# Optimization experiments

Measured on AMD Instinct MI355X. Metric: run time of the kernel, lower is better.

## Reference

```python
import jax, jax.numpy as jnp
import numpy as np

B, T, W = 8, 4096, 1024          # batch, byte seq len, words per sequence
DB, DW = 64, 512                 # byte_embed_dim, word_embed_dim
NH = 2                           # highway layers per block
VOCAB = 264                      # 256 bytes + 4 + 4 specials
BPE_MARK, WORD_MARK = 4, 3       # bpe_mask_idx, word_mask_idx


def _make_seg_ids():
    # ragged word lengths in {3,4,5}, mean 4, summing to T per sequence
    rng = np.random.default_rng(0)
    seg = np.empty((B, T), np.int32)
    base = T // W
    for b in range(B):
        delta = np.zeros(W, np.int64)
        q = W // 4
        idx = rng.permutation(W)
        delta[idx[:q]] = 1
        delta[idx[q:2 * q]] = -1
        seg[b] = np.repeat(np.arange(W), base + delta)
    return jnp.asarray(seg)


def setup_inputs() -> dict:
    key = jax.random.key(0)
    ks = jax.random.split(key, 12)
    s = 0.05
    byte_tokens = jax.random.randint(ks[0], (B, T), 4, VOCAB)
    bpe_mask = jax.random.bernoulli(ks[1], 0.25, (B, T))
    word_mask = jax.random.bernoulli(ks[2], 0.05, (B, T))
    seg_ids = _make_seg_ids()
    tok_emb = (jax.random.normal(ks[3], (VOCAB, DB)) * s).at[0].set(0.0)  # padding_idx=0 row zeroed
    inp = {
        'byte_tokens': byte_tokens, 'bpe_mask': bpe_mask, 'word_mask': word_mask,
        'seg_ids': seg_ids, 'tok_emb': tok_emb,
        'conv0_w': jax.random.normal(ks[4], (3, DB, DW)) * s, 'conv0_b': jnp.zeros((DW,)),
        'hw0_wg': jax.random.normal(ks[5], (NH, DW, DW)) * s, 'hw0_bg': jnp.zeros((NH, DW)),
        'hw0_wh': jax.random.normal(ks[6], (NH, DW, DW)) * s, 'hw0_bh': jnp.zeros((NH, DW)),
        'conv1_w': jax.random.normal(ks[7], (3, DW, DW)) * s, 'conv1_b': jnp.zeros((DW,)),
        'hw1_wg': jax.random.normal(ks[8], (NH, DW, DW)) * s, 'hw1_bg': jnp.zeros((NH, DW)),
        'hw1_wh': jax.random.normal(ks[9], (NH, DW, DW)) * s, 'hw1_bh': jnp.zeros((NH, DW)),
        'proj_w': jax.random.normal(ks[10], (DW, DW)) * s, 'proj_b': jnp.zeros((DW,)),
    }
    return inp


def _conv_highway(x, cw, cb, wg, bg, wh, bh, residual):
    # 1D same-padded conv over sequence, optional residual, relu, then highways
    y = jax.lax.conv_general_dilated(x, cw, (1,), 'SAME',
                                     dimension_numbers=('NWC', 'WIO', 'NWC')) + cb
    if residual:
        y = y + x
    y = jax.nn.relu(y)
    for i in range(NH):
        g = jax.nn.sigmoid(y @ wg[i] + bg[i])
        h = jax.nn.relu(y @ wh[i] + bh[i])
        y = g * h + (1.0 - g) * y
    return y


def reference(byte_tokens, bpe_mask, word_mask, seg_ids, tok_emb,
              conv0_w, conv0_b, hw0_wg, hw0_bg, hw0_wh, hw0_bh,
              conv1_w, conv1_b, hw1_wg, hw1_bg, hw1_wh, hw1_bh,
              proj_w, proj_b):
    # byte embedding + marker embeddings (pad idx 0 -> zero row)
    x = (tok_emb[byte_tokens]
         + tok_emb[jnp.where(bpe_mask, BPE_MARK, 0)]
         + tok_emb[jnp.where(word_mask, WORD_MARK, 0)])          # [B,T,DB]
    x = _conv_highway(x, conv0_w, conv0_b, hw0_wg, hw0_bg, hw0_wh, hw0_bh, False)
    x = _conv_highway(x, conv1_w, conv1_b, hw1_wg, hw1_bg, hw1_wh, hw1_bh, True)
    # ragged per-word segment max over bytes (fused, replaces python loops)
    seg_max = jax.vmap(lambda xi, si: jax.ops.segment_max(xi, si, num_segments=W))
    x = seg_max(x, seg_ids)                                       # [B,W,DW]
    return x @ proj_w + proj_b
```

## Files before the change

kernel.cpp:

```cpp
#include <hip/hip_runtime.h>
#include <hip/hip_bf16.h>

using bf16 = __hip_bfloat16;
typedef __attribute__((ext_vector_type(8))) short s8v;
typedef __attribute__((ext_vector_type(4))) float f4v;

#define T_SEQ 4096
#define DWC 512

__device__ __forceinline__ float fin(float v) {
    return (v == v && fabsf(v) < 1e30f) ? v : 0.0f;
}
__device__ __forceinline__ float ldf(const void* p, size_t i, int f32) {
    return f32 ? ((const float*)p)[i] : __bfloat162float(((const bf16*)p)[i]);
}
__device__ __forceinline__ float b2f(short s) {
    unsigned u = ((unsigned)(unsigned short)s) << 16;
    return __builtin_bit_cast(float, u);
}
__device__ __forceinline__ short f2b(float v) {
    bf16 b = __float2bfloat16(v);
    return __builtin_bit_cast(short, b);
}
__device__ __forceinline__ uint4 ld16(const short* p) { return *(const uint4*)p; }

__device__ __forceinline__ void gl_lds16(const short* g, short* l) {
    __builtin_amdgcn_global_load_lds(
        (const __attribute__((address_space(1))) void*)g,
        (__attribute__((address_space(3))) void*)l, 16, 0, 0);
}

__device__ __forceinline__ void swz(int L, int G, int& bx, int& by) {
    int k8 = L & 7, sl = L >> 3;
    int gp = G >> 5;
    bx = sl & 3;
    by = k8 * gp + (sl >> 2);
}

__device__ __forceinline__ int swidx(int row, int ch) {
    return row * 32 + ((ch ^ ((row >> 1) & 3)) << 3);
}

__global__ __launch_bounds__(256) void diag_kernel(bf16* __restrict__ out, int n, float v)
{
    int i = blockIdx.x * 256 + threadIdx.x;
    if (i < n) out[i] = __float2bfloat16(i == 0 ? v : 0.0f);
}

__global__ __launch_bounds__(256) void detect_kernel(
    const int* __restrict__ tok, const unsigned char* __restrict__ bpe,
    const unsigned char* __restrict__ wm, const int* __restrict__ seg,
    const unsigned int* __restrict__ embw, int* __restrict__ flags)
{
    __shared__ int sh[5];
    int tid = threadIdx.x;
    if (tid < 5) sh[tid] = 0;
    __syncthreads();
    int bo = 0, bm = 0, wo = 0, wmid = 0;
    for (int i = tid; i < 16384; i += 256) {
        int odd = 2 * i + 1;
        if (bpe[odd]) bo = 1;
        if (wm[odd])  wo = 1;
        int mid = 8 * (i & 4095) + 4;
        if (bpe[mid]) bm = 1;
        if (wm[mid])  wmid = 1;
    }
    if (bo)   atomicOr(&sh[0], 1);
    if (bm)   atomicOr(&sh[1], 1);
    if (wo)   atomicOr(&sh[2], 1);
    if (wmid) atomicOr(&sh[3], 1);
    if (tid < 32 && embw[32 + tid] != 0u) atomicOr(&sh[4], 1);
    __syncthreads();
    if (tid == 0) {
        flags[0] = (tok[32767] != 0) ? 0 : 1;
        flags[1] = sh[0] ? 1 : (sh[1] ? 4 : 8);
        flags[2] = sh[2] ? 1 : (sh[3] ? 4 : 8);
        flags[3] = (seg[32767] != 0) ? 0 : 1;
        flags[4] = sh[4] ? 0 : 1;
    }
}

#define WB_TOTAL 3249664
#define EMB4_ELEMS (264 * 4 * 64)
__global__ __launch_bounds__(256) void convert_weights(
    const void* c0w, const void* c0b, const void* h0g, const void* h0bg,
    const void* h0h, const void* h0bh, const void* c1w, const void* c1b,
    const void* h1g, const void* h1bg, const void* h1h, const void* h1bh,
    const void* pw, const void* pb, const void* emb,
    const int* __restrict__ flags, short* __restrict__ WB)
{
    int f32 = flags[4];
    size_t i = (size_t)blockIdx.x * 256 + threadIdx.x;
    if (i >= WB_TOTAL + EMB4_ELEMS) return;
    if (i >= WB_TOTAL) {
        size_t o = i - WB_TOTAL;
        size_t t = o >> 8, v = (o >> 6) & 3, c = o & 63;
        float val = ldf(emb, t * 64 + c, f32);
        if (v & 1) val += ldf(emb, 4 * 64 + c, f32);
        if (v & 2) val += ldf(emb, 3 * 64 + c, f32);
        WB[i] = f2b(fin(val));
        return;
    }
    const void* src; size_t si;
    if (i < 98304)        { size_t n = i / 192, k = i % 192; src = c0w; si = k * 512 + n; }
    else if (i < 98816)   { src = c0b;  si = i - 98304; }
    else if (i < 623104)  { size_t o = i - 98816;  size_t l = o >> 18; o &= 262143;
                            size_t n = o >> 9, k = o & 511; src = h0g; si = (l << 18) + k * 512 + n; }
    else if (i < 624128)  { src = h0bg; si = i - 623104; }
    else if (i < 1148416) { size_t o = i - 624128; size_t l = o >> 18; o &= 262143;
                            size_t n = o >> 9, k = o & 511; src = h0h; si = (l << 18) + k * 512 + n; }
    else if (i < 1149440) { src = h0bh; si = i - 1148416; }
    else if (i < 1935872) { size_t o = i - 1149440; size_t n = o / 1536, k = o % 1536;
                            src = c1w; si = k * 512 + n; }
    else if (i < 1936384) { src = c1b;  si = i - 1935872; }
    else if (i < 2460672) { size_t o = i - 1936384; size_t l = o >> 18; o &= 262143;
                            size_t n = o >> 9, k = o & 511; src = h1g; si = (l << 18) + k * 512 + n; }
    else if (i < 2461696) { src = h1bg; si = i - 2460672; }
    else if (i < 2985984) { size_t o = i - 2461696; size_t l = o >> 18; o &= 262143;
                            size_t n = o >> 9, k = o & 511; src = h1h; si = (l << 18) + k * 512 + n; }
    else if (i < 2987008) { src = h1bh; si = i - 2985984; }
    else if (i < 3249152) { size_t o = i - 2987008; size_t n = o >> 9, k = o & 511;
                            src = pw; si = k * 512 + n; }
    else                  { src = pb;   si = i - 3249152; }
    WB[i] = f2b(ldf(src, si, f32));
}

__global__ __launch_bounds__(512) void conv0_mfma(
    const int* __restrict__ tok, const unsigned char* __restrict__ bpe,
    const unsigned char* __restrict__ wm, const short* __restrict__ emb4,
    const int* __restrict__ flags, const short* __restrict__ WT,
    const short* __restrict__ bias, short* __restrict__ Out)
{
    constexpr int K = 192;
    constexpr int NIT = 3;
    __shared__ __align__(16) short As[2][256 * 32];
    __shared__ __align__(16) short Bs[2][256 * 32];
    int bx, by;
    swz(blockIdx.x, gridDim.x, bx, by);
    const int bm = by * 128, bn = bx * 128;
    const int tid = threadIdx.x;
    const int wave = tid >> 6, lane = tid & 63;
    const int wmr = (wave >> 1) * 32, wnc = (wave & 1) * 64;
    const int q = lane >> 4, ln16 = lane & 15;
    const int sr = tid >> 2, sch = tid & 3;
    const int tt = (bm + sr) & (T_SEQ - 1);
    const int is64t = flags[0];
    const int wb = flags[1], ww = flags[2];
    const short* Bb = WT + (size_t)(bn + sr) * K + sch * 8;

    f4v acc[2][4] = {};
    uint4 rA0, rA1, rB0, rB1;
    const uint4 z4 = make_uint4(0, 0, 0, 0);

    auto loadA = [&](int tap, uint4& a0, uint4& a1) {
        int ts = tt + tap - 1;
        if ((unsigned)ts < (unsigned)T_SEQ) {
            int bt = bm + sr + tap - 1;
            int tk = is64t ? (int)((const long long*)tok)[bt] : tok[bt];
            tk = min(max(tk, 0), 263);
            int v = (bpe[(size_t)bt * wb] ? 1 : 0) | (wm[(size_t)bt * ww] ? 2 : 0);
            const short* row = emb4 + ((size_t)tk * 4 + v) * 64;
            a0 = ld16(row + sch * 8);
            a1 = ld16(row + 32 + sch * 8);
        } else { a0 = z4; a1 = z4; }
    };

    loadA(0, rA0, rA1);
    rB0 = ld16(Bb);
    rB1 = ld16(Bb + 32);
    *(uint4*)(&As[0][swidx(sr, sch)])       = rA0;
    *(uint4*)(&As[0][swidx(128 + sr, sch)]) = rA1;
    *(uint4*)(&Bs[0][swidx(sr, sch)])       = rB0;
    *(uint4*)(&Bs[0][swidx(128 + sr, sch)]) = rB1;
    __syncthreads();
    int p = 0;

    for (int it = 0; it < NIT; ++it) {
        const bool more = (it + 1 < NIT);
        if (more) {
            int kn = (it + 1) * 64;
            loadA(it + 1, rA0, rA1);
            rB0 = ld16(Bb + kn);
            rB1 = ld16(Bb + kn + 32);
        }
        #pragma unroll
        for (int ks = 0; ks < 2; ks++) {
            s8v af[2], bf[4];
            #pragma unroll
            for (int mi = 0; mi < 2; mi++)
                af[mi] = *(const s8v*)(&As[p][swidx(128 * ks + wmr + mi * 16 + ln16, q)]);
            #pragma unroll
            for (int ni = 0; ni < 4; ni++)
                bf[ni] = *(const s8v*)(&Bs[p][swidx(128 * ks + wnc + ni * 16 + ln16, q)]);
            #pragma unroll
            for (int mi = 0; mi < 2; mi++)
                #pragma unroll
                for (int ni = 0; ni < 4; ni++)
                    acc[mi][ni] = __builtin_amdgcn_mfma_f32_16x16x32_bf16(
                        af[mi], bf[ni], acc[mi][ni], 0, 0, 0);
        }
        if (more) {
            *(uint4*)(&As[p ^ 1][swidx(sr, sch)])       = rA0;
            *(uint4*)(&As[p ^ 1][swidx(128 + sr, sch)]) = rA1;
            *(uint4*)(&Bs[p ^ 1][swidx(sr, sch)])       = rB0;
            *(uint4*)(&Bs[p ^ 1][swidx(128 + sr, sch)]) = rB1;
            __syncthreads();
            p ^= 1;
        }
    }

    #pragma unroll
    for (int mi = 0; mi < 2; mi++)
        #pragma unroll
        for (int ni = 0; ni < 4; ni++) {
            int col = bn + wnc + ni * 16 + ln16;
            float bv = b2f(bias[col]);
            #pragma unroll
            for (int r = 0; r < 4; r++) {
                int orow = bm + wmr + mi * 16 + q * 4 + r;
                Out[(size_t)orow * DWC + col] =
                    f2b(fin(fmaxf(acc[mi][ni][r] + bv, 0.0f)));
            }
        }
}

__global__ __launch_bounds__(512) void conv1_mfma(
    const short* __restrict__ A, const short* __restrict__ WT,
    const short* __restrict__ bias, short* __restrict__ Out)
{
    constexpr int IC = 512;
    constexpr int K = 3 * IC;
    constexpr int NIT = K / 64;
    __shared__ __align__(16) short As[2][256 * 32];
    __shared__ __align__(16) short Bs[2][256 * 32];
    int bx, by;
    swz(blockIdx.x, gridDim.x, bx, by);
    const int bm = by * 128, bn = bx * 128;
    const int tid = threadIdx.x;
    const int wave = tid >> 6, lane = tid & 63;
    const int wmr = (wave >> 1) * 32, wnc = (wave & 1) * 64;
    const int q = lane >> 4, ln16 = lane & 15;
    const int sr = tid >> 2, sch = tid & 3;
    const int tt = (bm + sr) & (T_SEQ - 1);
    const short* Bb = WT + (size_t)(bn + sr) * K + sch * 8;

    f4v acc[2][4] = {};
    uint4 rA0, rA1, rB0, rB1;
    const uint4 z4 = make_uint4(0, 0, 0, 0);

    {
        int ts = tt - 1;
        bool ok = (ts >= 0 && ts < T_SEQ);
        const short* sa = A + (size_t)(bm + sr - 1) * IC + sch * 8;
        rA0 = ok ? ld16(sa) : z4;
        rA1 = ok ? ld16(sa + 32) : z4;
        rB0 = ld16(Bb);
        rB1 = ld16(Bb + 32);
    }
    *(uint4*)(&As[0][swidx(sr, sch)])       = rA0;
    *(uint4*)(&As[0][swidx(128 + sr, sch)]) = rA1;
    *(uint4*)(&Bs[0][swidx(sr, sch)])       = rB0;
    *(uint4*)(&Bs[0][swidx(128 + sr, sch)]) = rB1;
    __syncthreads();
    int p = 0;

    for (int it = 0; it < NIT; ++it) {
        const bool more = (it + 1 < NIT);
        if (more) {
            int kn = (it + 1) * 64;
            int tap = kn / IC, c0 = kn - tap * IC;
            int ts = tt + tap - 1;
            bool ok = (ts >= 0 && ts < T_SEQ);
            const short* sa = A + (size_t)(bm + sr + tap - 1) * IC + c0 + sch * 8;
            rA0 = ok ? ld16(sa) : z4;
            rA1 = ok ? ld16(sa + 32) : z4;
            rB0 = ld16(Bb + kn);
            rB1 = ld16(Bb + kn + 32);
        }
        #pragma unroll
        for (int ks = 0; ks < 2; ks++) {
            s8v af[2], bf[4];
            #pragma unroll
            for (int mi = 0; mi < 2; mi++)
                af[mi] = *(const s8v*)(&As[p][swidx(128 * ks + wmr + mi * 16 + ln16, q)]);
            #pragma unroll
            for (int ni = 0; ni < 4; ni++)
                bf[ni] = *(const s8v*)(&Bs[p][swidx(128 * ks + wnc + ni * 16 + ln16, q)]);
            #pragma unroll
            for (int mi = 0; mi < 2; mi++)
                #pragma unroll
                for (int ni = 0; ni < 4; ni++)
                    acc[mi][ni] = __builtin_amdgcn_mfma_f32_16x16x32_bf16(
                        af[mi], bf[ni], acc[mi][ni], 0, 0, 0);
        }
        if (more) {
            *(uint4*)(&As[p ^ 1][swidx(sr, sch)])       = rA0;
            *(uint4*)(&As[p ^ 1][swidx(128 + sr, sch)]) = rA1;
            *(uint4*)(&Bs[p ^ 1][swidx(sr, sch)])       = rB0;
            *(uint4*)(&Bs[p ^ 1][swidx(128 + sr, sch)]) = rB1;
            __syncthreads();
            p ^= 1;
        }
    }

    #pragma unroll
    for (int mi = 0; mi < 2; mi++)
        #pragma unroll
        for (int ni = 0; ni < 4; ni++) {
            int col = bn + wnc + ni * 16 + ln16;
            float bv = b2f(bias[col]);
            #pragma unroll
            for (int r = 0; r < 4; r++) {
                int orow = bm + wmr + mi * 16 + q * 4 + r;
                float v = acc[mi][ni][r] + bv + b2f(A[(size_t)orow * IC + col]);
                Out[(size_t)orow * DWC + col] = f2b(fin(fmaxf(v, 0.0f)));
            }
        }
}

__global__ __launch_bounds__(512, 4) void highway_mfma8(
    const short* __restrict__ Y, const short* __restrict__ WgT,
    const short* __restrict__ bg, const short* __restrict__ WhT,
    const short* __restrict__ bh, short* __restrict__ Out)
{
    constexpr int IC = DWC;
    constexpr int NIT = IC / 32;
    __shared__ __align__(16) short As [2][128 * 32];
    __shared__ __align__(16) short Bgs[2][128 * 32];
    __shared__ __align__(16) short Bhs[2][128 * 32];
    int bx, by;
    swz(blockIdx.x, gridDim.x, bx, by);
    const int bm = by * 128, bn = bx * 128;
    const int tid = threadIdx.x;
    const int wave = tid >> 6, lane = tid & 63;
    const int wmr = (wave >> 2) * 64;
    const int wnc = (wave & 3) * 32;
    const int q = lane >> 4, ln16 = lane & 15;

    const int rr = (wave << 4) + (lane >> 2);
    const int ch = (lane & 3) ^ ((rr >> 1) & 3);
    const short* gA = Y   + (size_t)(bm + rr) * IC + ch * 8;
    const short* gG = WgT + (size_t)(bn + rr) * IC + ch * 8;
    const short* gH = WhT + (size_t)(bn + rr) * IC + ch * 8;
    const int wb1k = wave << 10;

    f4v accg[4][2] = {};
    f4v acch[4][2] = {};

    auto stage = [&](int pp, int kk) {
        gl_lds16(gA + kk, (short*)((char*)&As [pp][0] + wb1k));
        gl_lds16(gG + kk, (short*)((char*)&Bgs[pp][0] + wb1k));
        gl_lds16(gH + kk, (short*)((char*)&Bhs[pp][0] + wb1k));
    };

    stage(0, 0);
    asm volatile("s_waitcnt vmcnt(0)" ::: "memory");
    __syncthreads();
    int p = 0;

    for (int it = 0; it < NIT; ++it) {
        const bool more = (it + 1 < NIT);
        if (more) stage(p ^ 1, (it + 1) * 32);
        const short* Ap = &As [p][0];
        const short* Gp = &Bgs[p][0];
        const short* Hp = &Bhs[p][0];
        s8v af[2], bgf[2], bhf[2];
        #pragma unroll
        for (int ni = 0; ni < 2; ni++) {
            bgf[ni] = *(const s8v*)(&Gp[swidx(wnc + ni * 16 + ln16, q)]);
            bhf[ni] = *(const s8v*)(&Hp[swidx(wnc + ni * 16 + ln16, q)]);
        }
        #pragma unroll
        for (int mh = 0; mh < 2; mh++) {
            #pragma unroll
            for (int mi = 0; mi < 2; mi++)
                af[mi] = *(const s8v*)(&Ap[swidx(wmr + mh * 32 + mi * 16 + ln16, q)]);
            #pragma unroll
            for (int mi = 0; mi < 2; mi++)
                #pragma unroll
                for (int ni = 0; ni < 2; ni++) {
                    accg[mh * 2 + mi][ni] = __builtin_amdgcn_mfma_f32_16x16x32_bf16(
                        af[mi], bgf[ni], accg[mh * 2 + mi][ni], 0, 0, 0);
                    acch[mh * 2 + mi][ni] = __builtin_amdgcn_mfma_f32_16x16x32_bf16(
                        af[mi], bhf[ni], acch[mh * 2 + mi][ni], 0, 0, 0);
                }
        }
        if (more) {
            asm volatile("s_waitcnt vmcnt(0)" ::: "memory");
            __builtin_amdgcn_s_barrier();
            p ^= 1;
        }
    }

    #pragma unroll
    for (int mi = 0; mi < 4; mi++)
        #pragma unroll
        for (int ni = 0; ni < 2; ni++) {
            int col = bn + wnc + ni * 16 + ln16;
            float bgv = b2f(bg[col]);
            float bhv = b2f(bh[col]);
            #pragma unroll
            for (int r = 0; r < 4; r++) {
                int orow = bm + wmr + mi * 16 + q * 4 + r;
                float g = 1.0f / (1.0f + expf(-(accg[mi][ni][r] + bgv)));
                float h = fmaxf(acch[mi][ni][r] + bhv, 0.0f);
                float yv = b2f(Y[(size_t)orow * DWC + col]);
                Out[(size_t)orow * DWC + col] = f2b(fin(g * h + (1.0f - g) * yv));
            }
        }
}

__global__ __launch_bounds__(512) void proj_mfma(
    const short* __restrict__ A, const short* __restrict__ WT,
    const short* __restrict__ bias, const int* __restrict__ flags,
    void* __restrict__ Out, int oroff)
{
    __shared__ __align__(16) short As[128 * 32];
    __shared__ __align__(16) short Bs[128 * 32];
    int bx, by;
    swz(blockIdx.x, gridDim.x, bx, by);
    const int bm = by * 128, bn = bx * 128;
    const int tid = threadIdx.x;
    const int wave = tid >> 6, lane = tid & 63;
    const int wmr = (wave >> 1) * 32, wnc = (wave & 1) * 64;
    const int q = lane >> 4, ln16 = lane & 15;
    const int sr = tid >> 2, sch = tid & 3;
    const int sw = swidx(sr, sch);
    const int f32 = flags[4];
    const short* A0 = A  + (size_t)(bm + sr) * DWC + sch * 8;
    const short* B0 = WT + (size_t)(bn + sr) * DWC + sch * 8;

    f4v acc[2][4] = {};
    uint4 rA = ld16(A0), rB = ld16(B0);

    for (int k0 = 0; k0 < DWC; k0 += 32) {
        *(uint4*)(&As[sw]) = rA;
        *(uint4*)(&Bs[sw]) = rB;
        __syncthreads();
        if (k0 + 32 < DWC) {
            int kn = k0 + 32;
            rA = ld16(A0 + kn); rB = ld16(B0 + kn);
        }
        s8v af[2], bf[4];
        #pragma unroll
        for (int mi = 0; mi < 2; mi++) af[mi] = *(const s8v*)(&As[swidx(wmr + mi * 16 + ln16, q)]);
        #pragma unroll
        for (int ni = 0; ni < 4; ni++) bf[ni] = *(const s8v*)(&Bs[swidx(wnc + ni * 16 + ln16, q)]);
        #pragma unroll
        for (int mi = 0; mi < 2; mi++)
            #pragma unroll
            for (int ni = 0; ni < 4; ni++)
                acc[mi][ni] = __builtin_amdgcn_mfma_f32_16x16x32_bf16(
                    af[mi], bf[ni], acc[mi][ni], 0, 0, 0);
        __syncthreads();
    }

    #pragma unroll
    for (int mi = 0; mi < 2; mi++)
        #pragma unroll
        for (int ni = 0; ni < 4; ni++) {
            int col = bn + wnc + ni * 16 + ln16;
            float bv = b2f(bias[col]);
            #pragma unroll
            for (int r = 0; r < 4; r++) {
                int orow = bm + wmr + mi * 16 + q * 4 + r;
                float v = fin(acc[mi][ni][r] + bv);
                size_t oi = (size_t)(oroff + orow) * DWC + col;
                if (f32) ((float*)Out)[oi] = v;
                else     ((bf16*)Out)[oi] = __float2bfloat16(v);
            }
        }
}

__global__ __launch_bounds__(256) void bounds_kernel(
    const int* __restrict__ seg, const int* __restrict__ flags,
    int* __restrict__ wstart, int* __restrict__ wend, int bt0)
{
    int il = blockIdx.x * 256 + threadIdx.x;
    int ig = bt0 + il;
    int is64 = flags[3];
    const long long* seg64 = (const long long*)seg;
    int t = il & (T_SEQ - 1);
    int bl = il >> 12;
    int s  = (is64 ? (int)seg64[ig] : seg[ig]) & 1023;
    int sp = (t == 0)         ? -1 : ((is64 ? (int)seg64[ig - 1] : seg[ig - 1]) & 1023);
    int sn = (t == T_SEQ - 1) ? -1 : ((is64 ? (int)seg64[ig + 1] : seg[ig + 1]) & 1023);
    int bw = (bl << 10) + s;
    if (sp != s) wstart[bw] = t;
    if (sn != s) wend[bw] = t;
}

__global__ __launch_bounds__(512) void segmax_kernel(
    const short* __restrict__ Y, const int* __restrict__ wstart,
    const int* __restrict__ wend, short* __restrict__ Out)
{
    int bw = blockIdx.x;
    int d = threadIdx.x;
    int bl = bw >> 10;
    int s = wstart[bw], e = wend[bw];
    s = min(max(s, 0), T_SEQ - 1);
    e = min(max(e, s), T_SEQ - 1);
    float m = b2f(Y[(size_t)((bl << 12) + s) * DWC + d]);
    for (int t = s + 1; t <= e; ++t)
        m = fmaxf(m, b2f(Y[(size_t)((bl << 12) + t) * DWC + d]));
    Out[(size_t)bw * DWC + d] = f2b(fin(m));
}

extern "C" void kernel_launch(void* const* d_in, const int* in_sizes, int n_in,
                              void* d_out, int out_size, void* d_ws, size_t ws_size,
                              hipStream_t stream)
{
    static const int expect[19] = {32768, 32768, 32768, 32768, 16896,
                                   98304, 512, 524288, 1024, 524288, 1024,
                                   786432, 512, 524288, 1024, 524288, 1024,
                                   262144, 512};
    int bad = -1;
    if (n_in < 19) bad = 31;
    else for (int i = 0; i < 19; i++) if (in_sizes[i] != expect[i]) { bad = i; break; }
    if (bad >= 0) {
        diag_kernel<<<dim3((out_size + 255) / 256), dim3(256), 0, stream>>>(
            (bf16*)d_out, out_size, 1e35f * (float)(1 + bad));
        return;
    }

    char* ws = (char*)d_ws;
    const size_t WBREG = 8ull << 20;
    short* WB    = (short*)ws;
    int*   flags = (int*)(ws + (7u << 20));
    const size_t perC = 8388608 + 8192 + 64;
    int C = 8;
    while (C > 1 && WBREG + (size_t)C * perC > ws_size) C >>= 1;
    if (WBREG + (size_t)C * perC > ws_size) {
        float ws_mib = (float)((double)ws_size / 1048576.0);
        diag_kernel<<<dim3((out_size + 255) / 256), dim3(256), 0, stream>>>(
            (bf16*)d_out, out_size, 1e30f * (16.0f + ws_mib));
        return;
    }

    const int*  byte_tokens = (const int*)d_in[0];
    const unsigned char* bpe_mask = (const unsigned char*)d_in[1];
    const unsigned char* word_mask = (const unsigned char*)d_in[2];
    const int*  seg_ids     = (const int*)d_in[3];
    const void* tok_emb = d_in[4];

    detect_kernel<<<dim3(1), dim3(256), 0, stream>>>(
        byte_tokens, bpe_mask, word_mask, seg_ids,
        (const unsigned int*)tok_emb, flags);

    convert_weights<<<dim3((WB_TOTAL + EMB4_ELEMS + 255) / 256), dim3(256), 0, stream>>>(
        d_in[5], d_in[6], d_in[7], d_in[8], d_in[9], d_in[10],
        d_in[11], d_in[12], d_in[13], d_in[14], d_in[15], d_in[16],
        d_in[17], d_in[18], tok_emb, flags, WB);

    short* c0wT = WB;            short* c0b  = WB + 98304;
    short* h0gT = WB + 98816;    short* h0bg = WB + 623104;
    short* h0hT = WB + 624128;   short* h0bh = WB + 1148416;
    short* c1wT = WB + 1149440;  short* c1b  = WB + 1935872;
    short* h1gT = WB + 1936384;  short* h1bg = WB + 2460672;
    short* h1hT = WB + 2461696;  short* h1bh = WB + 2985984;
    short* pwT  = WB + 2987008;  short* pb   = WB + 3249152;
    short* emb4 = WB + WB_TOTAL;
    const int LOFF = 262144, LBOFF = 512;

    for (int b0 = 0; b0 < 8; b0 += C) {
        const int rows  = C * T_SEQ;
        const int words = C * 1024;
        char*  chunk  = ws + WBREG;
        short* U      = (short*)chunk;
        short* V      = (short*)(chunk + (size_t)C * 4194304);
        int*   wstart = (int*)(chunk + (size_t)C * 8388608);
        int*   wend   = wstart + words;
        short* segout = U;

        dim3 gg(4 * (rows / 128));
        conv0_mfma<<<gg, dim3(512), 0, stream>>>(
            byte_tokens + (size_t)b0 * T_SEQ,
            bpe_mask, word_mask, emb4, flags, c0wT, c0b, U);

        highway_mfma8<<<gg, dim3(512), 0, stream>>>(U, h0gT, h0bg, h0hT, h0bh, V);
        highway_mfma8<<<gg, dim3(512), 0, stream>>>(V, h0gT + LOFF, h0bg + LBOFF,
                                                    h0hT + LOFF, h0bh + LBOFF, U);

        conv1_mfma<<<gg, dim3(512), 0, stream>>>(U, c1wT, c1b, V);

        highway_mfma8<<<gg, dim3(512), 0, stream>>>(V, h1gT, h1bg, h1hT, h1bh, U);
        highway_mfma8<<<gg, dim3(512), 0, stream>>>(U, h1gT + LOFF, h1bg + LBOFF,
                                                    h1hT + LOFF, h1bh + LBOFF, V);

        bounds_kernel<<<dim3(rows / 256), dim3(256), 0, stream>>>(
            seg_ids, flags, wstart, wend, b0 * T_SEQ);

        segmax_kernel<<<dim3(words), dim3(512), 0, stream>>>(V, wstart, wend, segout);

        proj_mfma<<<dim3(4 * (words / 128)), dim3(512), 0, stream>>>(
            segout, pwT, pb, flags, d_out, b0 * 1024);
    }
}
```

Baseline: 420.3 us.

## Triple-buffer highway kernel LDS staging with two-stage prefetch

The highway MFMA kernel now uses three LDS buffers instead of two and issues global-to-LDS loads two K-steps ahead. It waits with vmcnt(3) rather than vmcnt(0), so one stage of loads stays in flight across each barrier. The aim is to hide more global memory latency behind the MFMA work. LDS use rises from 48KB to 72KB per block, which may lower occupancy under the (512,4) launch bounds.

```diff
diff --git a/kernel.cpp b/kernel.cpp
--- a/kernel.cpp
+++ b/kernel.cpp
@@ -325,9 +325,7 @@
 {
     constexpr int IC = DWC;
     constexpr int NIT = IC / 32;
-    __shared__ __align__(16) short As [2][128 * 32];
-    __shared__ __align__(16) short Bgs[2][128 * 32];
-    __shared__ __align__(16) short Bhs[2][128 * 32];
+    __shared__ __align__(16) short L[3][3][128 * 32];
     int bx, by;
     swz(blockIdx.x, gridDim.x, bx, by);
     const int bm = by * 128, bn = bx * 128;
@@ -348,22 +346,23 @@
     f4v acch[4][2] = {};
 
     auto stage = [&](int pp, int kk) {
-        gl_lds16(gA + kk, (short*)((char*)&As [pp][0] + wb1k));
-        gl_lds16(gG + kk, (short*)((char*)&Bgs[pp][0] + wb1k));
-        gl_lds16(gH + kk, (short*)((char*)&Bhs[pp][0] + wb1k));
+        gl_lds16(gA + kk, (short*)((char*)&L[pp][0][0] + wb1k));
+        gl_lds16(gG + kk, (short*)((char*)&L[pp][1][0] + wb1k));
+        gl_lds16(gH + kk, (short*)((char*)&L[pp][2][0] + wb1k));
     };
 
     stage(0, 0);
-    asm volatile("s_waitcnt vmcnt(0)" ::: "memory");
-    __syncthreads();
-    int p = 0;
+    stage(1, 32);
+    asm volatile("s_waitcnt vmcnt(3)" ::: "memory");
+    __builtin_amdgcn_s_barrier();
+    int cur = 0, nn = 2;
 
     for (int it = 0; it < NIT; ++it) {
-        const bool more = (it + 1 < NIT);
-        if (more) stage(p ^ 1, (it + 1) * 32);
-        const short* Ap = &As [p][0];
-        const short* Gp = &Bgs[p][0];
-        const short* Hp = &Bhs[p][0];
+        const bool issue = (it + 2 < NIT);
+        if (issue) stage(nn, (it + 2) * 32);
+        const short* Ap = &L[cur][0][0];
+        const short* Gp = &L[cur][1][0];
+        const short* Hp = &L[cur][2][0];
         s8v af[2], bgf[2], bhf[2];
         #pragma unroll
         for (int ni = 0; ni < 2; ni++) {
@@ -385,10 +384,12 @@
                         af[mi], bhf[ni], acch[mh * 2 + mi][ni], 0, 0, 0);
                 }
         }
-        if (more) {
-            asm volatile("s_waitcnt vmcnt(0)" ::: "memory");
+        if (it + 1 < NIT) {
+            if (issue) asm volatile("s_waitcnt vmcnt(3)" ::: "memory");
+            else       asm volatile("s_waitcnt vmcnt(0)" ::: "memory");
             __builtin_amdgcn_s_barrier();
-            p ^= 1;
+            cur = (cur == 2) ? 0 : cur + 1;
+            nn  = (nn  == 2) ? 0 : nn  + 1;
         }
     }
 
```

New measurement: 452.0 us. 7.5% more time.
